# Kernel optimization log

Measured on AMD Instinct MI355X. Metric: run time of the kernel, lower is better.

## Reference

```python
import jax, jax.numpy as jnp
import numpy as np

B, S, ID = 4, 1024, 4096
R, RP, H, D = 512, 64, 32, 128  # lora_rank, rope_dim, n_heads, head_dim
EPS = 1.1920929e-07  # torch nn.RMSNorm default eps = finfo(float32).eps


def rms_norm(x, w):
    return x * jax.lax.rsqrt(jnp.mean(x * x, axis=-1, keepdims=True) + EPS) * w


def rope(x, cos_half, sin_half):
    # half/half pairing rotation (HF style)
    cos = jnp.concatenate([cos_half, cos_half], axis=-1)
    sin = jnp.concatenate([sin_half, sin_half], axis=-1)
    half = x.shape[-1] // 2
    rot = jnp.concatenate([-x[..., half:], x[..., :half]], axis=-1)
    return x * cos + rot * sin


def setup_inputs() -> dict:
    key = jax.random.key(0)
    ks = jax.random.split(key, 12)
    sc = 0.02
    x = jax.random.normal(ks[0], (B, S, ID), jnp.float32)
    # real RoPE tables, shape (S, RP//2)
    inv_freq = 1.0 / (10000.0 ** (jnp.arange(0, RP, 2, dtype=jnp.float32) / RP))
    ang = jnp.arange(S, dtype=jnp.float32)[:, None] * inv_freq[None, :]
    cos_half = jnp.cos(ang)
    sin_half = jnp.sin(ang)
    mask = jnp.zeros((S, S), jnp.float32)  # additive mask; no softmax in module so keep finite
    return {
        "x": x,
        "cos_half": cos_half,
        "sin_half": sin_half,
        "mask": mask,
        "w_dkv_kr_w": jax.random.normal(ks[1], (R + RP, ID), jnp.float32) * sc,
        "w_dkv_kr_b": jnp.zeros((R + RP,), jnp.float32),
        "kv_norm_w": jnp.ones((R,), jnp.float32),
        "w_dq_w": jax.random.normal(ks[2], (R, ID), jnp.float32) * sc,
        "w_dq_b": jnp.zeros((R,), jnp.float32),
        "q_norm_w": jnp.ones((R,), jnp.float32),
        "w_uq_w": jax.random.normal(ks[3], (H * D, R), jnp.float32) * sc,
        "w_uq_b": jnp.zeros((H * D,), jnp.float32),
        "w_qr_w": jax.random.normal(ks[4], (RP, R), jnp.float32) * sc,
        "w_qr_b": jnp.zeros((RP,), jnp.float32),
        "w_uk_w": jax.random.normal(ks[5], (H * D, R), jnp.float32) * sc,
        "w_uv_w": jax.random.normal(ks[6], (H * D, R), jnp.float32) * sc,
        "w_o_w": jax.random.normal(ks[7], (ID, H * D), jnp.float32) * sc,
        "w_o_b": jnp.zeros((ID,), jnp.float32),
        "start_pos": 0,
    }


def reference(x, cos_half, sin_half, mask, w_dkv_kr_w, w_dkv_kr_b, kv_norm_w,
              w_dq_w, w_dq_b, q_norm_w, w_uq_w, w_uq_b, w_qr_w, w_qr_b,
              w_uk_w, w_uv_w, w_o_w, w_o_b, start_pos):
    b, s, _ = x.shape
    # KV down-projection + decoupled rope key
    dkv = x @ w_dkv_kr_w.T + w_dkv_kr_b                      # (b,s,R+RP)
    c_kv = rms_norm(dkv[..., :R], kv_norm_w)                 # (b,s,R) == kv_cache[:,start:end] (start_pos=0, prefill)
    k_r = rope(dkv[..., R:], cos_half, sin_half)             # (b,s,RP) == pe_cache slice
    # Q path
    c_q = rms_norm(x @ w_dq_w.T + w_dq_b, q_norm_w)          # (b,s,R)
    q = (c_q @ w_uq_w.T + w_uq_b).reshape(b, s, H, D)        # (b,s,h,d)
    q_r = rope(c_q @ w_qr_w.T + w_qr_b, cos_half, sin_half)  # (b,s,RP)
    # weight absorption: fold w_uk into the query
    qW = jnp.einsum('bshd,hdr->bshr', q, w_uk_w.reshape(H, D, R))
    scores = jnp.einsum('bshr,btr->bsht', qW, c_kv)
    scores = scores + jnp.einsum('bsd,btd->bst', q_r, k_r)[:, :, None, :]
    scores = scores + mask[:, None, :]                       # (s,1,t) broadcast over (b,s,h,t)
    # NOTE: faithful to source -- no softmax / no scaling applied
    a_sum = jnp.einsum('bsht,btr->bshr', scores, c_kv)
    out = jnp.einsum('bshr,hdr->bshd', a_sum, w_uv_w.reshape(H, D, R))
    out = out.reshape(b, s, H * D)
    return out @ w_o_w.T + w_o_b
```

## Files before the change

### kernel.cpp

```cpp
#include <hip/hip_runtime.h>
#include <hip/hip_bf16.h>

typedef __attribute__((ext_vector_type(8))) short s8v;
typedef __attribute__((ext_vector_type(4))) float f4v;
typedef __hip_bfloat16 bf16;

#define BSZ 4
#define SEQ 1024
#define IDIM 4096
#define RNK 512
#define RPD 64
#define NH 32
#define HD 128
#define BT 4096

__device__ __forceinline__ void load_lds16(const bf16* g, bf16* l) {
  __builtin_amdgcn_global_load_lds((const __attribute__((address_space(1))) void*)g,
                                   (__attribute__((address_space(3))) void*)l, 16, 0, 0);
}

template<int OUT_BF16, int HAS_BIAS>
__global__ __launch_bounds__(512, 2) void gemm256(
    const bf16* __restrict__ A, const bf16* __restrict__ B, void* __restrict__ Cv,
    const float* __restrict__ bias, int K, int lda, int ldb, int ldc, int NXT)
{
  __shared__ bf16 As[2][256 * 64];
  __shared__ bf16 Bs[2][256 * 64];

  int nwg = gridDim.x, orig = blockIdx.x, cpx = nwg >> 3;
  int l = (orig & 7) * cpx + (orig >> 3);
  int tx = l % NXT, ty = l / NXT;
  long long rowBase = (long long)ty * 256;
  long long colBase = (long long)tx * 256;

  int tid = threadIdx.x, lane = tid & 63, wave = tid >> 6;
  int wr = wave >> 2, wc = wave & 3;
  int lrow = lane & 15, lslot = lane >> 4;
  int NT = K >> 6;

  int srow = tid >> 3, sslot = tid & 7;
  int skc = sslot ^ (srow & 7);
  int sdst = srow * 64 + sslot * 8;
  const bf16* aP0 = A + (rowBase + srow      ) * lda + (skc << 3);
  const bf16* aP1 = A + (rowBase + srow +  64) * lda + (skc << 3);
  const bf16* aP2 = A + (rowBase + srow + 128) * lda + (skc << 3);
  const bf16* aP3 = A + (rowBase + srow + 192) * lda + (skc << 3);
  const bf16* bP0 = B + (colBase + srow      ) * ldb + (skc << 3);
  const bf16* bP1 = B + (colBase + srow +  64) * ldb + (skc << 3);
  const bf16* bP2 = B + (colBase + srow + 128) * ldb + (skc << 3);
  const bf16* bP3 = B + (colBase + srow + 192) * ldb + (skc << 3);

#define SG_A(bs, dk, i) load_lds16(aP##i + (dk) * 64, &As[bs][sdst + (i) * 4096])
#define SG_B(bs, dk, i) load_lds16(bP##i + (dk) * 64, &Bs[bs][sdst + (i) * 4096])

  int offk0 = ((lslot ^ (lrow & 7)) << 3);
  int offk1 = (((4 | lslot) ^ (lrow & 7)) << 3);
  int aoff = (wr * 128 + lrow) * 64;
  int boff = (wc * 64 + lrow) * 64;

  f4v acc[8][4];
  #pragma unroll
  for (int m = 0; m < 8; ++m)
    #pragma unroll
    for (int n = 0; n < 4; ++n) acc[m][n] = {0.f, 0.f, 0.f, 0.f};

#define PHASE(BSEL, Q, STG, GATE) do {                                         \
    const bf16* Ab_ = &As[BSEL][aoff];                                         \
    s8v a00 = *(const s8v*)(Ab_ + (2*(Q))   * 1024 + offk0);                   \
    s8v a01 = *(const s8v*)(Ab_ + (2*(Q))   * 1024 + offk1);                   \
    s8v a10 = *(const s8v*)(Ab_ + (2*(Q)+1) * 1024 + offk0);                   \
    s8v a11 = *(const s8v*)(Ab_ + (2*(Q)+1) * 1024 + offk1);                   \
    if ((Q) == 0) {                                                            \
      const bf16* Bb_ = &Bs[BSEL][boff];                                       \
      _Pragma("unroll")                                                        \
      for (int n = 0; n < 4; ++n) {                                            \
        b0[n] = *(const s8v*)(Bb_ + n * 1024 + offk0);                         \
        b1[n] = *(const s8v*)(Bb_ + n * 1024 + offk1);                         \
      }                                                                        \
    }                                                                          \
    STG;                                                                       \
    asm volatile("s_barrier" ::: "memory");                                    \
    __builtin_amdgcn_s_setprio(1);                                             \
    _Pragma("unroll")                                                          \
    for (int n = 0; n < 4; ++n)                                                \
      acc[2*(Q)][n]   = __builtin_amdgcn_mfma_f32_16x16x32_bf16(a00, b0[n], acc[2*(Q)][n], 0, 0, 0);   \
    _Pragma("unroll")                                                          \
    for (int n = 0; n < 4; ++n)                                                \
      acc[2*(Q)+1][n] = __builtin_amdgcn_mfma_f32_16x16x32_bf16(a10, b0[n], acc[2*(Q)+1][n], 0, 0, 0); \
    _Pragma("unroll")                                                          \
    for (int n = 0; n < 4; ++n)                                                \
      acc[2*(Q)][n]   = __builtin_amdgcn_mfma_f32_16x16x32_bf16(a01, b1[n], acc[2*(Q)][n], 0, 0, 0);   \
    _Pragma("unroll")                                                          \
    for (int n = 0; n < 4; ++n)                                                \
      acc[2*(Q)+1][n] = __builtin_amdgcn_mfma_f32_16x16x32_bf16(a11, b1[n], acc[2*(Q)+1][n], 0, 0, 0); \
    __builtin_amdgcn_s_setprio(0);                                             \
    GATE;                                                                      \
    asm volatile("s_barrier" ::: "memory");                                    \
  } while (0)

  SG_B(0, 0, 0); SG_B(0, 0, 1); SG_B(0, 0, 2); SG_B(0, 0, 3);
  SG_A(0, 0, 0); SG_A(0, 0, 1); SG_A(0, 0, 2); SG_A(0, 0, 3);
  SG_B(1, 1, 0); SG_B(1, 1, 1); SG_B(1, 1, 2); SG_B(1, 1, 3);
  SG_A(1, 1, 0); SG_A(1, 1, 2);
  asm volatile("s_waitcnt vmcnt(6)" ::: "memory");
  asm volatile("s_barrier" ::: "memory");

  for (int u = 0; u < NT; u += 2) {
    bool st2 = (u + 2 < NT);
    s8v b0[4], b1[4];
    PHASE(0, 0, { SG_A(1, 1, 1); SG_A(1, 1, 3); }, {});
    PHASE(0, 1, { if (st2) { SG_B(0, 2, 0); SG_B(0, 2, 1); } }, {});
    PHASE(0, 2, { if (st2) { SG_B(0, 2, 2); SG_B(0, 2, 3); } }, {});
    PHASE(0, 3, { if (st2) { SG_A(0, 2, 0); SG_A(0, 2, 2); } },
          { if (st2) asm volatile("s_waitcnt vmcnt(6)" ::: "memory");
            else     asm volatile("s_waitcnt vmcnt(0)" ::: "memory"); });
    PHASE(1, 0, { if (st2) { SG_A(0, 2, 1); SG_A(0, 2, 3); } }, {});
    PHASE(1, 1, { if (st2) { SG_B(1, 3, 0); SG_B(1, 3, 1); } }, {});
    PHASE(1, 2, { if (st2) { SG_B(1, 3, 2); SG_B(1, 3, 3); } }, {});
    PHASE(1, 3, { if (st2) { SG_A(1, 3, 0); SG_A(1, 3, 2); } },
          { if (st2) asm volatile("s_waitcnt vmcnt(6)" ::: "memory"); });
    aP0 += 128; aP1 += 128; aP2 += 128; aP3 += 128;
    bP0 += 128; bP1 += 128; bP2 += 128; bP3 += 128;
  }
#undef PHASE
#undef SG_A
#undef SG_B

  float* Cf = (float*)Cv;
  bf16* Cb = (bf16*)Cv;
  int lcol = lane & 15, lr4 = (lane >> 4) * 4;
  #pragma unroll
  for (int m = 0; m < 8; ++m)
    #pragma unroll
    for (int n = 0; n < 4; ++n) {
      long long col = colBase + wc * 64 + n * 16 + lcol;
      float bv_ = HAS_BIAS ? bias[col] : 0.f;
      #pragma unroll
      for (int j = 0; j < 4; ++j) {
        long long row = rowBase + wr * 128 + m * 16 + lr4 + j;
        float v = acc[m][n][j] + bv_;
        if (OUT_BF16) Cb[row * ldc + col] = __float2bfloat16(v);
        else          Cf[row * ldc + col] = v;
      }
    }
}

template<int BM, int BN, int WTM, int WTN, int OUT_BF16, int ADD_MODE, int HAS_BIAS>
__global__ __launch_bounds__(256) void gemm_bt(
    const bf16* __restrict__ A, const bf16* __restrict__ B, void* __restrict__ Cv,
    const float* __restrict__ bias, const void* __restrict__ addend,
    int K, int lda, int ldb, int ldc, int ldadd, int nz2,
    long long sA1, long long sA2, long long sB1, long long sB2,
    long long sC1, long long sC2, long long sD1, long long sD2)
{
  constexpr int BK = 32;
  constexpr int WM = BM / WTM, WN = BN / WTN;
  constexpr int FM = WM / 16, FN = WN / 16;
  static_assert(WTM * WTN == 4, "4 waves / 256 threads");
  static_assert((BM * BK) % 2048 == 0 && (BN * BK) % 2048 == 0, "staging coverage");
  __shared__ alignas(16) bf16 As[BM * BK];
  __shared__ alignas(16) bf16 Bs[BN * BK];

  int z = blockIdx.z;
  int z1 = z / nz2, z2 = z - z1 * nz2;
  A += z1 * sA1 + z2 * sA2;
  B += z1 * sB1 + z2 * sB2;
  long long coff = z1 * sC1 + z2 * sC2;
  long long doffz = z1 * sD1 + z2 * sD2;

  int tid = threadIdx.x;
  int lane = tid & 63, wave = tid >> 6;
  int wr = wave / WTN, wc = wave % WTN;
  int rowBase = blockIdx.y * BM;
  int colBase = blockIdx.x * BN;

  f4v acc[FM][FN];
  #pragma unroll
  for (int i = 0; i < FM; ++i)
    #pragma unroll
    for (int j = 0; j < FN; ++j) acc[i][j] = {0.f, 0.f, 0.f, 0.f};

  constexpr int A_LOADS = (BM * BK) / 2048;
  constexpr int B_LOADS = (BN * BK) / 2048;
  int lrow = lane & 15;
  int rsw = (lrow >> 1) & 3;
  int lkA = ((lane >> 4) ^ rsw) * 8;

  for (int k0 = 0; k0 < K; k0 += BK) {
    #pragma unroll
    for (int i = 0; i < A_LOADS; ++i) {
      int e = tid * 8 + i * 2048;
      int r_ = e >> 5, sp_ = (e >> 3) & 3, kc_ = sp_ ^ ((r_ >> 1) & 3);
      load_lds16(A + (long long)(rowBase + r_) * lda + k0 + (kc_ << 3), &As[e]);
    }
    #pragma unroll
    for (int i = 0; i < B_LOADS; ++i) {
      int e = tid * 8 + i * 2048;
      int r_ = e >> 5, sp_ = (e >> 3) & 3, kc_ = sp_ ^ ((r_ >> 1) & 3);
      load_lds16(B + (long long)(colBase + r_) * ldb + k0 + (kc_ << 3), &Bs[e]);
    }
    __syncthreads();

    s8v av[FM], bv[FN];
    #pragma unroll
    for (int fm = 0; fm < FM; ++fm)
      av[fm] = *(const s8v*)&As[(wr * WM + fm * 16 + lrow) * BK + lkA];
    #pragma unroll
    for (int fn = 0; fn < FN; ++fn)
      bv[fn] = *(const s8v*)&Bs[(wc * WN + fn * 16 + lrow) * BK + lkA];
    #pragma unroll
    for (int fm = 0; fm < FM; ++fm)
      #pragma unroll
      for (int fn = 0; fn < FN; ++fn)
        acc[fm][fn] = __builtin_amdgcn_mfma_f32_16x16x32_bf16(av[fm], bv[fn], acc[fm][fn], 0, 0, 0);
    __syncthreads();
  }

  bf16* Cb = (bf16*)Cv;
  float* Cf = (float*)Cv;
  const float* addf = (const float*)addend;
  const bf16* addb = (const bf16*)addend;
  int lcol = lane & 15, lr4 = (lane >> 4) * 4;
  #pragma unroll
  for (int fm = 0; fm < FM; ++fm) {
    #pragma unroll
    for (int fn = 0; fn < FN; ++fn) {
      int col = colBase + wc * WN + fn * 16 + lcol;
      #pragma unroll
      for (int j = 0; j < 4; ++j) {
        int row = rowBase + wr * WM + fm * 16 + lr4 + j;
        float v = acc[fm][fn][j];
        if (HAS_BIAS) v += bias[col];
        if (ADD_MODE == 1) v += addf[doffz + (long long)row * ldadd + col];
        if (ADD_MODE == 2) v += __bfloat162float(addb[doffz + (long long)row * ldadd + col]);
        long long idx = coff + (long long)row * ldc + col;
        if (OUT_BF16) Cb[idx] = __float2bfloat16(v);
        else          Cf[idx] = v;
      }
    }
  }
}


__global__ void cast4(const float* __restrict__ in, bf16* __restrict__ out, int n4) {
  int i = blockIdx.x * 256 + threadIdx.x;
  if (i >= n4) return;
  float4 v = ((const float4*)in)[i];
  union { ushort4 u; bf16 h[4]; } o;
  o.h[0] = __float2bfloat16(v.x); o.h[1] = __float2bfloat16(v.y);
  o.h[2] = __float2bfloat16(v.z); o.h[3] = __float2bfloat16(v.w);
  ((ushort4*)out)[i] = o.u;
}

struct CastJobs {
  const float* s[8];
  bf16* d[8];
  int n4[8];
  int b0[8];
};
__global__ __launch_bounds__(256) void cast_multi(CastJobs J) {
  int blk = blockIdx.x, j = 0;
  #pragma unroll
  for (int k = 1; k < 8; ++k) if (blk >= J.b0[k]) j = k;
  int i = (blk - J.b0[j]) * 256 + threadIdx.x;
  if (i >= J.n4[j]) return;
  float4 v = ((const float4*)J.s[j])[i];
  union { ushort4 u; bf16 h[4]; } o;
  o.h[0] = __float2bfloat16(v.x); o.h[1] = __float2bfloat16(v.y);
  o.h[2] = __float2bfloat16(v.z); o.h[3] = __float2bfloat16(v.w);
  ((ushort4*)J.d[j])[i] = o.u;
}

__global__ __launch_bounds__(256) void tr_bf16(const bf16* __restrict__ in, bf16* __restrict__ out,
                                               int R, int C) {
  __shared__ bf16 t[32][33];
  long long zo = (long long)blockIdx.z * R * C;
  int c0 = blockIdx.x * 32, r0 = blockIdx.y * 32;
  int tx = threadIdx.x & 31, ty = threadIdx.x >> 5;
  #pragma unroll
  for (int i = 0; i < 32; i += 8)
    t[ty + i][tx] = in[zo + (long long)(r0 + ty + i) * C + (c0 + tx)];
  __syncthreads();
  #pragma unroll
  for (int i = 0; i < 32; i += 8)
    out[zo + (long long)(c0 + ty + i) * R + (r0 + tx)] = t[tx][ty + i];
}

__device__ __forceinline__ float block_sum256(float v) {
  #pragma unroll
  for (int o = 32; o > 0; o >>= 1) v += __shfl_xor(v, o, 64);
  __shared__ float red[4];
  int lane = threadIdx.x & 63, w = threadIdx.x >> 6;
  if (lane == 0) red[w] = v;
  __syncthreads();
  return red[0] + red[1] + red[2] + red[3];
}

__global__ __launch_bounds__(256) void rms_dkv(const float* __restrict__ dq,
    const float* __restrict__ w, const float* __restrict__ ch, const float* __restrict__ sh,
    bf16* __restrict__ ckv, bf16* __restrict__ kr) {
  int row = blockIdx.x, t = threadIdx.x;
  const float* xr = dq + (long long)row * 1088;
  float v0 = xr[t], v1 = xr[t + 256];
  float ss = block_sum256(v0 * v0 + v1 * v1);
  float sc = rsqrtf(ss * (1.0f / 512.0f) + 1.1920929e-07f);
  long long o = (long long)row * 512;
  ckv[o + t]       = __float2bfloat16(v0 * sc * w[t]);
  ckv[o + t + 256] = __float2bfloat16(v1 * sc * w[t + 256]);
  if (t < 64) {
    int s = row & (SEQ - 1);
    float a = xr[512 + t], r;
    if (t < 32) r = a * ch[s * 32 + t]      - xr[512 + t + 32] * sh[s * 32 + t];
    else        r = a * ch[s * 32 + t - 32] + xr[512 + t - 32] * sh[s * 32 + t - 32];
    kr[(long long)row * 64 + t] = __float2bfloat16(r);
  }
}

__global__ __launch_bounds__(256) void rms512(const float* __restrict__ dq,
    const float* __restrict__ w, bf16* __restrict__ out) {
  int row = blockIdx.x, t = threadIdx.x;
  const float* xr = dq + (long long)row * 1088 + 576;
  float v0 = xr[t], v1 = xr[t + 256];
  float ss = block_sum256(v0 * v0 + v1 * v1);
  float sc = rsqrtf(ss * (1.0f / 512.0f) + 1.1920929e-07f);
  long long o = (long long)row * 512;
  out[o + t]       = __float2bfloat16(v0 * sc * w[t]);
  out[o + t + 256] = __float2bfloat16(v1 * sc * w[t + 256]);
}

__global__ void rope_qr(const float* __restrict__ in, const float* __restrict__ ch,
                        const float* __restrict__ sh, bf16* __restrict__ out) {
  int row = blockIdx.x, t = threadIdx.x;
  const float* xr = in + (long long)row * 64;
  int s = row & (SEQ - 1);
  float a = xr[t], r;
  if (t < 32) r = a * ch[s * 32 + t]      - xr[t + 32] * sh[s * 32 + t];
  else        r = a * ch[s * 32 + t - 32] + xr[t - 32] * sh[s * 32 + t - 32];
  out[(long long)row * 64 + t] = __float2bfloat16(r);
}

extern "C" void kernel_launch(void* const* d_in, const int* in_sizes, int n_in,
                              void* d_out, int out_size, void* d_ws, size_t ws_size,
                              hipStream_t stream) {
  const float* x    = (const float*)d_in[0];
  const float* ch   = (const float*)d_in[1];
  const float* sh   = (const float*)d_in[2];
  const float* mask = (const float*)d_in[3];
  const float* wdkv = (const float*)d_in[4];
  const float* bdkv = (const float*)d_in[5];
  const float* kvnw = (const float*)d_in[6];
  const float* wdq  = (const float*)d_in[7];
  const float* bdq  = (const float*)d_in[8];
  const float* qnw  = (const float*)d_in[9];
  const float* wuq  = (const float*)d_in[10];
  const float* buq  = (const float*)d_in[11];
  const float* wqr  = (const float*)d_in[12];
  const float* bqr  = (const float*)d_in[13];
  const float* wuk  = (const float*)d_in[14];
  const float* wuv  = (const float*)d_in[15];
  const float* wo   = (const float*)d_in[16];
  const float* bo   = (const float*)d_in[17];
  float* out = (float*)d_out;
  (void)in_sizes; (void)n_in; (void)out_size; (void)ws_size;

  char* ws = (char*)d_ws;
  bf16* regionA = (bf16*)(ws);
  bf16* outh    = (bf16*)(ws + 33554432);
  bf16* wdkv_b  = (bf16*)(ws + 67108864);
  bf16* wdq_b   = (bf16*)(ws + 71827456);
  bf16* wuq_b   = (bf16*)(ws + 76021760);
  bf16* wqr_b   = (bf16*)(ws + 80216064);
  bf16* wuv_b   = (bf16*)(ws + 80281600);
  bf16* wuk_b   = (bf16*)(ws + 84475904);
  bf16* mask_b  = (bf16*)(ws + 88670208);
  char* regionB = ws + 90767360;
  float* dq_cat = (float*)(regionB);
  bf16* Eb      = (bf16*)(regionB);
  bf16* FT      = (bf16*)(regionB + 16777216);

  bf16* xb   = regionA;
  bf16* wo_b = regionA;

  char* ob = (char*)d_out;
  bf16* qb     = (bf16*)(ob);
  char* U      = ob + 33554432;
  bf16* ckv    = (bf16*)(U);
  bf16* kr     = (bf16*)(U + 4194304);
  bf16* ckvT   = (bf16*)(U + 4718592);
  bf16* krT    = (bf16*)(U + 8912896);
  bf16* cq     = (bf16*)(U + 9437184);
  float* qr_pre= (float*)(U + 13631488);
  bf16* qr_b   = (bf16*)(U + 14680064);
  bf16* Gm     = (bf16*)(U + 15204352);
  bf16* Mt     = (bf16*)(U + 17301504);
  bf16* base_b = (bf16*)(U + 17563648);

  float* bias_cat = qr_pre;

  long long Z = 0;

  {
    CastJobs J;
    const float* srcs[8] = {x, wdkv, wdq, wqr, mask, wuq, wuv, wuk};
    bf16* dsts[8] = {xb, wdkv_b, wdq_b, wqr_b, mask_b, wuq_b, wuv_b, wuk_b};
    int n4s[8] = {4194304, 589824, 524288, 8192, 262144, 524288, 524288, 524288};
    int accb = 0;
    for (int j = 0; j < 8; ++j) {
      J.s[j] = srcs[j]; J.d[j] = dsts[j]; J.n4[j] = n4s[j];
      J.b0[j] = accb; accb += (n4s[j] + 255) / 256;
    }
    cast_multi<<<dim3(accb), 256, 0, stream>>>(J);
  }
  hipMemcpyAsync(bias_cat, bdkv, 576 * 4, hipMemcpyDeviceToDevice, stream);
  hipMemcpyAsync(bias_cat + 576, bdq, 512 * 4, hipMemcpyDeviceToDevice, stream);

  gemm_bt<128, 64, 4, 1, 0, 0, 1><<<dim3(17, 32, 1), 256, 0, stream>>>(
      xb, wdkv_b, dq_cat, bias_cat, nullptr, 4096, 4096, 4096, 1088, 0, 1, Z,Z,Z,Z,Z,Z,Z,Z);
  rms_dkv<<<dim3(BT), 256, 0, stream>>>(dq_cat, kvnw, ch, sh, ckv, kr);
  rms512<<<dim3(BT), 256, 0, stream>>>(dq_cat, qnw, cq);
  tr_bf16<<<dim3(16, 32, 4), 256, 0, stream>>>(ckv, ckvT, 1024, 512);
  tr_bf16<<<dim3(2, 32, 4), 256, 0, stream>>>(kr, krT, 1024, 64);

  cast4<<<dim3(16384), 256, 0, stream>>>(wo, wo_b, 4194304);

  gemm256<1, 1><<<dim3(256), 512, 0, stream>>>(
      cq, wuq_b, qb, buq, 512, 512, 512, 4096, 16);

  gemm_bt<128, 64, 4, 1, 0, 0, 1><<<dim3(1, 32, 1), 256, 0, stream>>>(
      cq, wqr_b, qr_pre, bqr, nullptr, 512, 512, 512, 64, 0, 1, Z,Z,Z,Z,Z,Z,Z,Z);
  rope_qr<<<dim3(BT), 64, 0, stream>>>(qr_pre, ch, sh, qr_b);

  gemm_bt<128, 128, 2, 2, 1, 0, 0><<<dim3(4, 4, 4), 256, 0, stream>>>(
      ckvT, ckvT, Gm, nullptr, nullptr, 1024, 1024, 1024, 512, 0, 1,
      524288LL, Z, 524288LL, Z, 262144LL, Z, Z, Z);

  gemm_bt<128, 64, 4, 1, 1, 0, 0><<<dim3(1, 4, 4), 256, 0, stream>>>(
      ckvT, krT, Mt, nullptr, nullptr, 1024, 1024, 1024, 64, 0, 1,
      524288LL, Z, 65536LL, Z, 32768LL, Z, Z, Z);

  gemm_bt<128, 128, 2, 2, 1, 0, 0><<<dim3(4, 8, 4), 256, 0, stream>>>(
      mask_b, ckvT, base_b, nullptr, nullptr, 1024, 1024, 1024, 512, 0, 1,
      Z, Z, 524288LL, Z, 524288LL, Z, Z, Z);

  gemm_bt<128, 128, 2, 2, 1, 2, 0><<<dim3(4, 8, 4), 256, 0, stream>>>(
      qr_b, Mt, base_b, nullptr, base_b, 64, 64, 64, 512, 512, 1,
      65536LL, Z, 32768LL, Z, 524288LL, Z, 524288LL, Z);

  gemm256<1, 0><<<dim3(256), 512, 0, stream>>>(
      base_b, wuv_b, outh, nullptr, 512, 512, 512, 4096, 16);

  gemm_bt<128, 128, 2, 2, 1, 0, 0><<<dim3(4, 1, 128), 256, 0, stream>>>(
      wuv_b, Gm, Eb, nullptr, nullptr, 512, 512, 512, 512, 0, 32,
      Z, 65536LL, 262144LL, Z, 2097152LL, 65536LL, Z, Z);

  gemm_bt<128, 128, 2, 2, 1, 0, 0><<<dim3(1, 1, 128), 256, 0, stream>>>(
      Eb, wuk_b, FT, nullptr, nullptr, 512, 512, 512, 128, 0, 32,
      2097152LL, 65536LL, Z, 65536LL, 524288LL, 16384LL, Z, Z);

  gemm_bt<128, 128, 2, 2, 1, 2, 0><<<dim3(1, 8, 128), 256, 0, stream>>>(
      qb, FT, outh, nullptr, outh, 128, 4096, 128, 4096, 4096, 32,
      4194304LL, 128LL, 524288LL, 16384LL, 4194304LL, 128LL, 4194304LL, 128LL);

  gemm256<0, 1><<<dim3(256), 512, 0, stream>>>(
      outh, wo_b, out, bo, 4096, 4096, 4096, 4096, 16);
}
```

Baseline: 457.3 us.

## Pad fused down-projection to 1152 columns with 128x128 tiles and reorder gemm256 prefetch

Concatenates the KV and Q down-projection weights into one contiguous buffer padded with zero rows to 1152 outputs. The fused x projection can then use a 128x128 tiled GEMM config (9x32 grid) instead of 128x64 tiles over 1088 columns. The consumer row stride changes to match. The gemm256 main loop is also rescheduled so full A tiles load before B tiles, with the vmcnt wait threshold lowered from 6 to 4. In exchange the padding adds wasted compute and two memsets per call.

```diff
diff --git a/kernel.cpp b/kernel.cpp
--- a/kernel.cpp
+++ b/kernel.cpp
@@ -98,27 +98,26 @@
     asm volatile("s_barrier" ::: "memory");                                    \
   } while (0)
 
+  SG_A(0, 0, 0); SG_A(0, 0, 1); SG_A(0, 0, 2); SG_A(0, 0, 3);
   SG_B(0, 0, 0); SG_B(0, 0, 1); SG_B(0, 0, 2); SG_B(0, 0, 3);
-  SG_A(0, 0, 0); SG_A(0, 0, 1); SG_A(0, 0, 2); SG_A(0, 0, 3);
   SG_B(1, 1, 0); SG_B(1, 1, 1); SG_B(1, 1, 2); SG_B(1, 1, 3);
-  SG_A(1, 1, 0); SG_A(1, 1, 2);
-  asm volatile("s_waitcnt vmcnt(6)" ::: "memory");
+  asm volatile("s_waitcnt vmcnt(4)" ::: "memory");
   asm volatile("s_barrier" ::: "memory");
 
   for (int u = 0; u < NT; u += 2) {
-    bool st2 = (u + 2 < NT);
+    bool st = (u + 2 < NT);
     s8v b0[4], b1[4];
-    PHASE(0, 0, { SG_A(1, 1, 1); SG_A(1, 1, 3); }, {});
-    PHASE(0, 1, { if (st2) { SG_B(0, 2, 0); SG_B(0, 2, 1); } }, {});
-    PHASE(0, 2, { if (st2) { SG_B(0, 2, 2); SG_B(0, 2, 3); } }, {});
-    PHASE(0, 3, { if (st2) { SG_A(0, 2, 0); SG_A(0, 2, 2); } },
-          { if (st2) asm volatile("s_waitcnt vmcnt(6)" ::: "memory");
-            else     asm volatile("s_waitcnt vmcnt(0)" ::: "memory"); });
-    PHASE(1, 0, { if (st2) { SG_A(0, 2, 1); SG_A(0, 2, 3); } }, {});
-    PHASE(1, 1, { if (st2) { SG_B(1, 3, 0); SG_B(1, 3, 1); } }, {});
-    PHASE(1, 2, { if (st2) { SG_B(1, 3, 2); SG_B(1, 3, 3); } }, {});
-    PHASE(1, 3, { if (st2) { SG_A(1, 3, 0); SG_A(1, 3, 2); } },
-          { if (st2) asm volatile("s_waitcnt vmcnt(6)" ::: "memory"); });
+    PHASE(0, 0, { SG_A(1, 1, 0); SG_A(1, 1, 1); }, {});
+    PHASE(0, 1, { SG_A(1, 1, 2); SG_A(1, 1, 3); }, {});
+    PHASE(0, 2, { if (st) { SG_B(0, 2, 0); SG_B(0, 2, 1); } }, {});
+    PHASE(0, 3, { if (st) { SG_B(0, 2, 2); SG_B(0, 2, 3); } },
+          { if (st) asm volatile("s_waitcnt vmcnt(4)" ::: "memory");
+            else    asm volatile("s_waitcnt vmcnt(0)" ::: "memory"); });
+    PHASE(1, 0, { if (st) { SG_A(0, 2, 0); SG_A(0, 2, 1); } }, {});
+    PHASE(1, 1, { if (st) { SG_A(0, 2, 2); SG_A(0, 2, 3); } }, {});
+    PHASE(1, 2, { if (st) { SG_B(1, 3, 0); SG_B(1, 3, 1); } }, {});
+    PHASE(1, 3, { if (st) { SG_B(1, 3, 2); SG_B(1, 3, 3); } },
+          { if (st) asm volatile("s_waitcnt vmcnt(4)" ::: "memory"); });
     aP0 += 128; aP1 += 128; aP2 += 128; aP3 += 128;
     bP0 += 128; bP1 += 128; bP2 += 128; bP3 += 128;
   }
@@ -300,7 +299,7 @@
     const float* __restrict__ w, const float* __restrict__ ch, const float* __restrict__ sh,
     bf16* __restrict__ ckv, bf16* __restrict__ kr) {
   int row = blockIdx.x, t = threadIdx.x;
-  const float* xr = dq + (long long)row * 1088;
+  const float* xr = dq + (long long)row * 1152;
   float v0 = xr[t], v1 = xr[t + 256];
   float ss = block_sum256(v0 * v0 + v1 * v1);
   float sc = rsqrtf(ss * (1.0f / 512.0f) + 1.1920929e-07f);
@@ -319,7 +318,7 @@
 __global__ __launch_bounds__(256) void rms512(const float* __restrict__ dq,
     const float* __restrict__ w, bf16* __restrict__ out) {
   int row = blockIdx.x, t = threadIdx.x;
-  const float* xr = dq + (long long)row * 1088 + 576;
+  const float* xr = dq + (long long)row * 1152 + 576;
   float v0 = xr[t], v1 = xr[t + 256];
   float ss = block_sum256(v0 * v0 + v1 * v1);
   float sc = rsqrtf(ss * (1.0f / 512.0f) + 1.1920929e-07f);
@@ -366,14 +365,13 @@
   char* ws = (char*)d_ws;
   bf16* regionA = (bf16*)(ws);
   bf16* outh    = (bf16*)(ws + 33554432);
-  bf16* wdkv_b  = (bf16*)(ws + 67108864);
-  bf16* wdq_b   = (bf16*)(ws + 71827456);
-  bf16* wuq_b   = (bf16*)(ws + 76021760);
-  bf16* wqr_b   = (bf16*)(ws + 80216064);
-  bf16* wuv_b   = (bf16*)(ws + 80281600);
-  bf16* wuk_b   = (bf16*)(ws + 84475904);
-  bf16* mask_b  = (bf16*)(ws + 88670208);
-  char* regionB = ws + 90767360;
+  bf16* wcat_b  = (bf16*)(ws + 67108864);
+  bf16* wuq_b   = (bf16*)(ws + 76546048);
+  bf16* wqr_b   = (bf16*)(ws + 80740352);
+  bf16* wuv_b   = (bf16*)(ws + 80805888);
+  bf16* wuk_b   = (bf16*)(ws + 85000192);
+  bf16* mask_b  = (bf16*)(ws + 89194496);
+  char* regionB = ws + 91291648;
   float* dq_cat = (float*)(regionB);
   bf16* Eb      = (bf16*)(regionB);
   bf16* FT      = (bf16*)(regionB + 16777216);
@@ -399,10 +397,11 @@
 
   long long Z = 0;
 
+  hipMemsetAsync(ws + 67108864 + 8912896, 0, 524288, stream);
   {
     CastJobs J;
     const float* srcs[8] = {x, wdkv, wdq, wqr, mask, wuq, wuv, wuk};
-    bf16* dsts[8] = {xb, wdkv_b, wdq_b, wqr_b, mask_b, wuq_b, wuv_b, wuk_b};
+    bf16* dsts[8] = {xb, wcat_b, wcat_b + 576 * 4096, wqr_b, mask_b, wuq_b, wuv_b, wuk_b};
     int n4s[8] = {4194304, 589824, 524288, 8192, 262144, 524288, 524288, 524288};
     int accb = 0;
     for (int j = 0; j < 8; ++j) {
@@ -411,11 +410,12 @@
     }
     cast_multi<<<dim3(accb), 256, 0, stream>>>(J);
   }
+  hipMemsetAsync(bias_cat, 0, 1152 * 4, stream);
   hipMemcpyAsync(bias_cat, bdkv, 576 * 4, hipMemcpyDeviceToDevice, stream);
   hipMemcpyAsync(bias_cat + 576, bdq, 512 * 4, hipMemcpyDeviceToDevice, stream);
 
-  gemm_bt<128, 64, 4, 1, 0, 0, 1><<<dim3(17, 32, 1), 256, 0, stream>>>(
-      xb, wdkv_b, dq_cat, bias_cat, nullptr, 4096, 4096, 4096, 1088, 0, 1, Z,Z,Z,Z,Z,Z,Z,Z);
+  gemm_bt<128, 128, 2, 2, 0, 0, 1><<<dim3(9, 32, 1), 256, 0, stream>>>(
+      xb, wcat_b, dq_cat, bias_cat, nullptr, 4096, 4096, 4096, 1152, 0, 1, Z,Z,Z,Z,Z,Z,Z,Z);
   rms_dkv<<<dim3(BT), 256, 0, stream>>>(dq_cat, kvnw, ch, sh, ckv, kr);
   rms512<<<dim3(BT), 256, 0, stream>>>(dq_cat, qnw, cq);
   tr_bf16<<<dim3(16, 32, 4), 256, 0, stream>>>(ckv, ckvT, 1024, 512);
```

Measured after the change: 485.6 us. +6.2%, slower.
